# Performance work log

Hardware: AMD Instinct MI355X
Metric: run time of the kernel (lower is better)

The kernel has to match this reference:

```python
import jax, jax.numpy as jnp
import numpy as np

B, RULE_DIM, E, P, TOP_K = 8192, 128, 64, 16, 3
EPS = 1e-5
CONF_THRESH = 0.1


def _ln(x, g, b):
    # torch.nn.LayerNorm: biased variance, eps=1e-5
    m = x.mean(-1, keepdims=True)
    v = ((x - m) ** 2).mean(-1, keepdims=True)
    return (x - m) / jnp.sqrt(v + EPS) * g + b


def setup_inputs() -> dict:
    key = jax.random.key(0)
    ks = jax.random.split(key, 8)
    s = lambda fan: 1.0 / np.sqrt(fan)
    return {
        "rule_embedding": jax.random.normal(ks[0], (B, RULE_DIM), jnp.float32),
        "rp_w1": jax.random.normal(ks[1], (RULE_DIM, 256), jnp.float32) * s(RULE_DIM),
        "rp_b1": jnp.zeros((256,), jnp.float32),
        "rp_g1": jnp.ones((256,), jnp.float32),
        "rp_be1": jnp.zeros((256,), jnp.float32),
        "rp_w2": jax.random.normal(ks[2], (256, 512), jnp.float32) * s(256),
        "rp_b2": jnp.zeros((512,), jnp.float32),
        "rp_g2": jnp.ones((512,), jnp.float32),
        "rp_be2": jnp.zeros((512,), jnp.float32),
        "op_w": jax.random.normal(ks[3], (512, E), jnp.float32) * s(512),
        "op_b": jnp.zeros((E,), jnp.float32),
        "pe_w1": jax.random.normal(ks[4], (E, 512, 256), jnp.float32) * s(512),
        "pe_b1": jnp.zeros((E, 256), jnp.float32),
        "pe_g": jnp.ones((E, 256), jnp.float32),
        "pe_beta": jnp.zeros((E, 256), jnp.float32),
        "pe_w2": jax.random.normal(ks[5], (E, 256, P), jnp.float32) * s(256),
        "pe_b2": jnp.zeros((E, P), jnp.float32),
    }


def reference(rule_embedding, rp_w1, rp_b1, rp_g1, rp_be1, rp_w2, rp_b2,
              rp_g2, rp_be2, op_w, op_b, pe_w1, pe_b1, pe_g, pe_beta,
              pe_w2, pe_b2):
    # rule_parser: Linear -> LN -> ReLU -> Linear -> LN -> ReLU
    h = jax.nn.relu(_ln(rule_embedding @ rp_w1 + rp_b1, rp_g1, rp_be1))   # [B,256]
    features = jax.nn.relu(_ln(h @ rp_w2 + rp_b2, rp_g2, rp_be2))         # [B,512]

    # op routing: softmax + top-k
    op_probs = jax.nn.softmax(features @ op_w + op_b, axis=-1)            # [B,E]
    top_probs, top_idx = jax.lax.top_k(op_probs, TOP_K)                   # [B,K]

    # per-op param predictor MLP, evaluated for every expert (vmap over E)
    def expert(w1, b1, g, be, w2, b2):
        z = jax.nn.relu(_ln(features @ w1 + b1, g, be))                   # [B,256]
        return z @ w2 + b2                                                # [B,P]

    h2_all = jax.vmap(expert)(pe_w1, pe_b1, pe_g, pe_beta, pe_w2, pe_b2)  # [E,B,P]

    # gather the selected expert's raw param logits per (token, slot)
    params_sel = h2_all[top_idx, jnp.arange(B)[:, None], :]               # [B,K,P]

    # original skips ops with confidence < 0.1 -> mask them out
    mask = (top_probs >= CONF_THRESH).astype(params_sel.dtype)            # [B,K]
    params_out = params_sel * mask[..., None]

    return top_probs, top_idx, params_out
```

## Files before the change

kernel.cpp:

```cpp
#include <hip/hip_runtime.h>
#include <math.h>

#define Bv   8192
#define EPSv 1e-5f
#define CONFv 0.1f
#define MB (1024*1024)

typedef __attribute__((ext_vector_type(8))) short short8;
typedef __attribute__((ext_vector_type(4))) float f32x4;

__device__ __forceinline__ float wave_sum64(float v){
  #pragma unroll
  for (int o = 32; o; o >>= 1) v += __shfl_xor(v, o, 64);
  return v;
}

__device__ __forceinline__ void split3f(float x, short &h, short &m, short &l){
  unsigned u = __float_as_uint(x);
  h = (short)(u >> 16);
  float r1 = x - __uint_as_float(u & 0xffff0000u);
  unsigned u1 = __float_as_uint(r1);
  m = (short)(u1 >> 16);
  float r2 = r1 - __uint_as_float(u1 & 0xffff0000u);
  l = (short)(__float_as_uint(r2) >> 16);
}

__device__ __forceinline__ void split2f(float x, short &h, short &m){
  unsigned u = __float_as_uint(x);
  h = (short)(u >> 16);
  float r1 = x - __uint_as_float(u & 0xffff0000u);
  m = (short)(__float_as_uint(r1) >> 16);
}

__device__ __forceinline__ f32x4 mfma5(short8 ah, short8 am,
                                       short8 bh, short8 bm, short8 bl, f32x4 c){
  c = __builtin_amdgcn_mfma_f32_16x16x32_bf16(am, bm, c, 0, 0, 0);
  c = __builtin_amdgcn_mfma_f32_16x16x32_bf16(ah, bl, c, 0, 0, 0);
  c = __builtin_amdgcn_mfma_f32_16x16x32_bf16(am, bh, c, 0, 0, 0);
  c = __builtin_amdgcn_mfma_f32_16x16x32_bf16(ah, bm, c, 0, 0, 0);
  c = __builtin_amdgcn_mfma_f32_16x16x32_bf16(ah, bh, c, 0, 0, 0);
  return c;
}

__device__ __forceinline__ f32x4 mfma3(short8 ah, short8 al,
                                       short8 bh, short8 bl, f32x4 c){
  c = __builtin_amdgcn_mfma_f32_16x16x32_bf16(al, bh, c, 0, 0, 0);
  c = __builtin_amdgcn_mfma_f32_16x16x32_bf16(ah, bl, c, 0, 0, 0);
  c = __builtin_amdgcn_mfma_f32_16x16x32_bf16(ah, bh, c, 0, 0, 0);
  return c;
}

__global__ __launch_bounds__(256) void k_pre(
    const float* __restrict__ w1, const float* __restrict__ w2,
    const float* __restrict__ opw,
    unsigned short* __restrict__ w1p, unsigned short* __restrict__ w2p,
    unsigned short* __restrict__ opwp, int* __restrict__ cnt)
{
  int bid = blockIdx.x;
  if (bid < 128){
    int gid = bid*256 + threadIdx.x;
    int k = gid >> 8, n = gid & 255;
    short h, m, l;
    split3f(w1[gid], h, m, l);
    int idx = (((n >> 4)*4 + (k >> 5))*64 + (((k >> 3) & 3)*16 + (n & 15)))*8 + (k & 7);
    w1p[idx]             = (unsigned short)h;
    w1p[32768 + idx]     = (unsigned short)m;
    w1p[2*32768 + idx]   = (unsigned short)l;
  } else if (bid < 640){
    int gid = (bid - 128)*256 + threadIdx.x;
    int k = gid >> 9, n = gid & 511;
    short h, m, l;
    split3f(w2[gid], h, m, l);
    int idx = (((n >> 4)*8 + (k >> 5))*64 + (((k >> 3) & 3)*16 + (n & 15)))*8 + (k & 7);
    w2p[idx]             = (unsigned short)h;
    w2p[131072 + idx]    = (unsigned short)m;
    w2p[2*131072 + idx]  = (unsigned short)l;
  } else if (bid < 768){
    int gid = (bid - 640)*256 + threadIdx.x;
    int k = gid >> 6, n = gid & 63;
    short h, m, l;
    split3f(opw[gid], h, m, l);
    int idx = (((n >> 4)*16 + (k >> 5))*64 + (((k >> 3) & 3)*16 + (n & 15)))*8 + (k & 7);
    opwp[idx]            = (unsigned short)h;
    opwp[32768 + idx]    = (unsigned short)m;
    opwp[2*32768 + idx]  = (unsigned short)l;
  } else {
    if (threadIdx.x < 64) cnt[threadIdx.x] = 0;
  }
}

__global__ __launch_bounds__(1024) void k_fused(const float* __restrict__ X,
    const unsigned short* __restrict__ w1p, const float* __restrict__ b1,
    const float* __restrict__ g1, const float* __restrict__ be1,
    const unsigned short* __restrict__ w2p, const float* __restrict__ b2,
    const float* __restrict__ g2, const float* __restrict__ be2,
    const unsigned short* __restrict__ opwp, const float* __restrict__ opb,
    unsigned short* __restrict__ fh, unsigned short* __restrict__ fl,
    float* __restrict__ dout, int* __restrict__ cnt, int* __restrict__ list,
    const float* __restrict__ pw1, const float* __restrict__ pw2,
    unsigned short* __restrict__ p1, unsigned short* __restrict__ p2)
{
  extern __shared__ unsigned char smem[];

  if (blockIdx.x >= 256){
    int pb = blockIdx.x - 256;
    if (pb < 1024){
      int t = pb*1024 + threadIdx.x;
      int e = t >> 14, rem = t & 16383, kg = rem >> 8, n = rem & 255;
      const float* src = pw1 + ((size_t)e << 17) + (size_t)(kg*8)*256 + n;
      short8 h, l;
      #pragma unroll
      for (int j = 0; j < 8; j++){
        float w = src[(size_t)j*256];
        unsigned u = __float_as_uint(w);
        float r2 = w - __uint_as_float(u & 0xffff0000u);
        h[j] = (short)(u >> 16);
        l[j] = (short)(__float_as_uint(r2) >> 16);
      }
      int idx8 = ((((n >> 4)*16 + (kg >> 2))*64) + (kg & 3)*16 + (n & 15)) << 3;
      unsigned short* ep = p1 + (size_t)e * 262144;
      *(short8*)(ep + idx8)          = h;
      *(short8*)(ep + 131072 + idx8) = l;
    } else {
      int t = (pb - 1024)*1024 + threadIdx.x;
      int e = t >> 9, rem = t & 511, kg = rem >> 4, n = rem & 15;
      const float* src = pw2 + (size_t)e*4096 + (size_t)(kg*8)*16 + n;
      short8 h, l;
      #pragma unroll
      for (int j = 0; j < 8; j++){
        float w = src[(size_t)j*16];
        unsigned u = __float_as_uint(w);
        float r2 = w - __uint_as_float(u & 0xffff0000u);
        h[j] = (short)(u >> 16);
        l[j] = (short)(__float_as_uint(r2) >> 16);
      }
      int idx8 = (((kg >> 2)*64) + (kg & 3)*16 + n) << 3;
      unsigned short* ep = p2 + (size_t)e * 8192;
      *(short8*)(ep + idx8)        = h;
      *(short8*)(ep + 4096 + idx8) = l;
    }
    return;
  }

  unsigned short* xh  = (unsigned short*)smem;
  unsigned short* xm  = xh + 4096;
  unsigned short* hbh = xh + 8192;
  unsigned short* hbm = xh + 16384;
  unsigned short* gah = xh;
  unsigned short* gam = xh + 16384;
  __shared__ float ps[32][20];
  __shared__ float pq[32][20];
  __shared__ float mi[32][2];
  __shared__ float lg[32][64];

  const int tid = threadIdx.x;
  const int r0  = blockIdx.x * 32;
  const int wave = tid >> 6, lane = tid & 63, lquad = lane >> 4, l15 = lane & 15;

  {
    int r = tid >> 5, c4 = tid & 31;
    float4 v = ((const float4*)X)[(size_t)(r0+r)*32 + c4];
    unsigned u0 = __float_as_uint(v.x), u1 = __float_as_uint(v.y);
    unsigned u2 = __float_as_uint(v.z), u3 = __float_as_uint(v.w);
    float m0 = v.x - __uint_as_float(u0 & 0xffff0000u);
    float m1 = v.y - __uint_as_float(u1 & 0xffff0000u);
    float m2 = v.z - __uint_as_float(u2 & 0xffff0000u);
    float m3 = v.w - __uint_as_float(u3 & 0xffff0000u);
    unsigned hp0 = (u0 >> 16) | (u1 & 0xffff0000u);
    unsigned hp1 = (u2 >> 16) | (u3 & 0xffff0000u);
    unsigned mp0 = (__float_as_uint(m0) >> 16) | (__float_as_uint(m1) & 0xffff0000u);
    unsigned mp1 = (__float_as_uint(m2) >> 16) | (__float_as_uint(m3) & 0xffff0000u);
    int gk = c4 >> 1, half = c4 & 1;
    int off = r*128 + ((gk ^ (r & 7)) << 3) + half*4;
    ((unsigned*)(xh + off))[0] = hp0;
    ((unsigned*)(xh + off))[1] = hp1;
    ((unsigned*)(xm + off))[0] = mp0;
    ((unsigned*)(xm + off))[1] = mp1;
  }
  __syncthreads();

  float bcol1, gcol1, becol1;
  {
    int col = wave*16 + l15;
    bcol1 = b1[col]; gcol1 = g1[col]; becol1 = be1[col];
  }
  {
    f32x4 acc[2];
    acc[0] = (f32x4){0.f,0.f,0.f,0.f};
    acc[1] = (f32x4){0.f,0.f,0.f,0.f};
    const int pstride = 32768;
    for (int ks4 = 0; ks4 < 4; ks4++){
      const unsigned short* bp = w1p + (((wave*4 + ks4)*64 + lane) << 3);
      short8 bh = *(const short8*)bp;
      short8 bm = *(const short8*)(bp + pstride);
      short8 bl = *(const short8*)(bp + 2*pstride);
      #pragma unroll
      for (int mt = 0; mt < 2; mt++){
        int r = mt*16 + l15;
        int off = r*128 + (((ks4*4 + lquad) ^ (r & 7)) << 3);
        short8 ah = *(const short8*)(xh + off);
        short8 am = *(const short8*)(xm + off);
        acc[mt] = mfma5(ah, am, bh, bm, bl, acc[mt]);
      }
    }
    #pragma unroll
    for (int mt = 0; mt < 2; mt++)
      #pragma unroll
      for (int reg = 0; reg < 4; reg++){
        float z = acc[mt][reg] + bcol1;
        float s = z, q = z*z;
        #pragma unroll
        for (int o = 1; o < 16; o <<= 1){ s += __shfl_xor(s, o, 64); q += __shfl_xor(q, o, 64); }
        int row = mt*16 + lquad*4 + reg;
        if (l15 == 0){ ps[row][wave] = s; pq[row][wave] = q; }
      }
    __syncthreads();
    if (tid < 32){
      int row = tid;
      float4 s0 = *(const float4*)&ps[row][0],  s1 = *(const float4*)&ps[row][4];
      float4 s2 = *(const float4*)&ps[row][8],  s3 = *(const float4*)&ps[row][12];
      float4 q0 = *(const float4*)&pq[row][0],  q1 = *(const float4*)&pq[row][4];
      float4 q2 = *(const float4*)&pq[row][8],  q3 = *(const float4*)&pq[row][12];
      float s = s0.x; s += s0.y; s += s0.z; s += s0.w;
      s += s1.x; s += s1.y; s += s1.z; s += s1.w;
      s += s2.x; s += s2.y; s += s2.z; s += s2.w;
      s += s3.x; s += s3.y; s += s3.z; s += s3.w;
      float q = q0.x; q += q0.y; q += q0.z; q += q0.w;
      q += q1.x; q += q1.y; q += q1.z; q += q1.w;
      q += q2.x; q += q2.y; q += q2.z; q += q2.w;
      q += q3.x; q += q3.y; q += q3.z; q += q3.w;
      float mean = s * (1.0f/256.0f);
      float var  = q * (1.0f/256.0f) - mean*mean;
      mi[row][0] = mean;
      mi[row][1] = 1.0f / sqrtf(var + EPSv);
    }
    __syncthreads();
    #pragma unroll
    for (int mt = 0; mt < 2; mt++)
      #pragma unroll
      for (int reg = 0; reg < 4; reg++){
        int row = mt*16 + lquad*4 + reg;
        float2 mv = *(const float2*)mi[row];
        int col = wave*16 + l15;
        float z = acc[mt][reg] + bcol1;
        float y = fmaxf((z - mv.x)*mv.y*gcol1 + becol1, 0.f);
        short hh, mm2;
        split2f(y, hh, mm2);
        int gg = col >> 3, c7 = col & 7;
        int adr = row*256 + ((gg ^ (row & 7)) << 3) + c7;
        hbh[adr] = (unsigned short)hh;
        hbm[adr] = (unsigned short)mm2;
      }
  }
  __syncthreads();

  f32x4 acc2[2][2];
  #pragma unroll
  for (int mt = 0; mt < 2; mt++)
    #pragma unroll
    for (int nt = 0; nt < 2; nt++) acc2[mt][nt] = (f32x4){0.f,0.f,0.f,0.f};
  {
    const int pstride = 131072;
    for (int ks4 = 0; ks4 < 8; ks4++){
      short8 ah[2], am[2];
      #pragma unroll
      for (int mt = 0; mt < 2; mt++){
        int r = mt*16 + l15;
        int off = r*256 + (((ks4*4 + lquad) ^ (r & 7)) << 3);
        ah[mt] = *(const short8*)(hbh + off);
        am[mt] = *(const short8*)(hbm + off);
      }
      #pragma unroll
      for (int nt = 0; nt < 2; nt++){
        int ntg = wave*2 + nt;
        const unsigned short* bp = w2p + (((ntg*8 + ks4)*64 + lane) << 3);
        short8 bh = *(const short8*)bp;
        short8 bm = *(const short8*)(bp + pstride);
        short8 bl = *(const short8*)(bp + 2*pstride);
        #pragma unroll
        for (int mt = 0; mt < 2; mt++)
          acc2[mt][nt] = mfma5(ah[mt], am[mt], bh, bm, bl, acc2[mt][nt]);
      }
    }
  }

  float bcol[2], gcol[2], becol[2];
  #pragma unroll
  for (int nt = 0; nt < 2; nt++){
    int col = (wave*2 + nt)*16 + l15;
    bcol[nt] = b2[col]; gcol[nt] = g2[col]; becol[nt] = be2[col];
  }
  #pragma unroll
  for (int mt = 0; mt < 2; mt++)
    #pragma unroll
    for (int reg = 0; reg < 4; reg++){
      float s = 0.f, q = 0.f;
      #pragma unroll
      for (int nt = 0; nt < 2; nt++){
        float z = acc2[mt][nt][reg] + bcol[nt];
        s += z; q += z*z;
      }
      #pragma unroll
      for (int o = 1; o < 16; o <<= 1){ s += __shfl_xor(s, o, 64); q += __shfl_xor(q, o, 64); }
      int row = mt*16 + lquad*4 + reg;
      if (l15 == 0){ ps[row][wave] = s; pq[row][wave] = q; }
    }
  __syncthreads();
  if (tid < 32){
    int row = tid;
    float4 s0 = *(const float4*)&ps[row][0],  s1 = *(const float4*)&ps[row][4];
    float4 s2 = *(const float4*)&ps[row][8],  s3 = *(const float4*)&ps[row][12];
    float4 q0 = *(const float4*)&pq[row][0],  q1 = *(const float4*)&pq[row][4];
    float4 q2 = *(const float4*)&pq[row][8],  q3 = *(const float4*)&pq[row][12];
    float s = s0.x; s += s0.y; s += s0.z; s += s0.w;
    s += s1.x; s += s1.y; s += s1.z; s += s1.w;
    s += s2.x; s += s2.y; s += s2.z; s += s2.w;
    s += s3.x; s += s3.y; s += s3.z; s += s3.w;
    float q = q0.x; q += q0.y; q += q0.z; q += q0.w;
    q += q1.x; q += q1.y; q += q1.z; q += q1.w;
    q += q2.x; q += q2.y; q += q2.z; q += q2.w;
    q += q3.x; q += q3.y; q += q3.z; q += q3.w;
    float mean = s * (1.0f/512.0f);
    float var  = q * (1.0f/512.0f) - mean*mean;
    mi[row][0] = mean;
    mi[row][1] = 1.0f / sqrtf(var + EPSv);
  }
  __syncthreads();

  #pragma unroll
  for (int mt = 0; mt < 2; mt++)
    #pragma unroll
    for (int reg = 0; reg < 4; reg++){
      int row = mt*16 + lquad*4 + reg;
      float2 mv = *(const float2*)mi[row];
      #pragma unroll
      for (int nt = 0; nt < 2; nt++){
        int col = (wave*2 + nt)*16 + l15;
        float z = acc2[mt][nt][reg] + bcol[nt];
        float y = fmaxf((z - mv.x)*mv.y*gcol[nt] + becol[nt], 0.f);
        short hh, mm2;
        split2f(y, hh, mm2);
        int gg = col >> 3, c7 = col & 7;
        int adr = row*512 + ((gg ^ (row & 7)) << 3) + c7;
        gah[adr] = (unsigned short)hh;
        gam[adr] = (unsigned short)mm2;
      }
    }
  __syncthreads();

  if (wave < 4){
    f32x4 accg[2];
    accg[0] = (f32x4){0.f,0.f,0.f,0.f};
    accg[1] = (f32x4){0.f,0.f,0.f,0.f};
    for (int kt = 0; kt < 16; kt++){
      const unsigned short* bp = opwp + (((wave*16 + kt)*64 + lane) << 3);
      short8 bh = *(const short8*)bp;
      short8 bm = *(const short8*)(bp + 32768);
      short8 bl = *(const short8*)(bp + 65536);
      #pragma unroll
      for (int mt = 0; mt < 2; mt++){
        int r = mt*16 + l15;
        int off = r*512 + (((kt*4 + lquad) ^ (r & 7)) << 3);
        short8 ah = *(const short8*)(gah + off);
        short8 am = *(const short8*)(gam + off);
        accg[mt] = mfma5(ah, am, bh, bm, bl, accg[mt]);
      }
    }
    float opbv = opb[wave*16 + l15];
    #pragma unroll
    for (int mt = 0; mt < 2; mt++)
      #pragma unroll
      for (int reg = 0; reg < 4; reg++)
        lg[mt*16 + lquad*4 + reg][wave*16 + l15] = accg[mt][reg] + opbv;
  } else {
    int t4 = (wave - 4)*64 + lane;
    for (int i = t4; i < 4096; i += 768){
      int p = i >> 11, rem = i & 2047, r = rem >> 6, gg = rem & 63;
      short8 v = *(const short8*)((p ? gam : gah) + r*512 + ((gg ^ (r & 7)) << 3));
      unsigned short* dst = (p ? fl : fh) + (size_t)(r0 + r)*512 + gg*8;
      *(short8*)dst = v;
    }
  }
  __syncthreads();

  {
    for (int rr = 0; rr < 2; rr++){
      int r = wave*2 + rr, row = r0 + r;
      float l = lg[r][lane];
      float mx = l;
      #pragma unroll
      for (int o = 32; o; o >>= 1) mx = fmaxf(mx, __shfl_xor(mx, o, 64));
      float p = expf(l - mx);
      float s = wave_sum64(p);
      p /= s;
      float pv = p;
      for (int j = 0; j < 3; j++){
        float v = pv; int idx = lane;
        #pragma unroll
        for (int o = 32; o; o >>= 1){
          float ov = __shfl_xor(v, o, 64);
          int   oi = __shfl_xor(idx, o, 64);
          if (ov > v || (ov == v && oi < idx)){ v = ov; idx = oi; }
        }
        if (lane == 0){
          dout[(size_t)row*3 + j]                = v;
          dout[(size_t)Bv*3 + (size_t)row*3 + j] = (float)idx;
        }
        if (v >= CONFv){
          if (lane == 0){
            int pos = atomicAdd(&cnt[idx], 1);
            list[idx*Bv + pos] = (row << 2) | j;
          }
        } else {
          if (lane < 16) dout[(size_t)Bv*6 + (size_t)row*48 + j*16 + lane] = 0.f;
        }
        if (lane == idx) pv = -1.0f;
      }
    }
  }
}

__global__ __launch_bounds__(512) void k_expert(const unsigned short* __restrict__ fh,
    const unsigned short* __restrict__ fl,
    const unsigned short* __restrict__ p1, const float* __restrict__ b1,
    const float* __restrict__ g,  const float* __restrict__ beta,
    const unsigned short* __restrict__ p2, const float* __restrict__ b2,
    const int* __restrict__ cnt,  const int* __restrict__ list,
    float* __restrict__ dout)
{
  extern __shared__ unsigned char smem[];
  unsigned short* xh = (unsigned short*)smem;
  unsigned short* xl = xh + 32*512;
  unsigned short* zp = (unsigned short*)smem;
  __shared__ float ps[32][12];
  __shared__ float pq[32][12];
  __shared__ float mi[32][2];
  __shared__ int sdesc[3];

  const int tid = threadIdx.x;
  const int wave = tid >> 6, lane = tid & 63;
  const int lquad = lane >> 4, l15 = lane & 15;

  if (wave == 0){
    int c  = cnt[lane];
    int tl = (c + 31) >> 5;
    int incl = tl;
    #pragma unroll
    for (int o = 1; o < 64; o <<= 1){
      int v = __shfl_up(incl, o, 64);
      if (lane >= o) incl += v;
    }
    int total = __shfl(incl, 63, 64);
    int G   = (total + 7) >> 3;
    int grp = blockIdx.x & 7, rr = blockIdx.x >> 3;
    int lgc = grp*G + rr;
    int ok  = (G > 0) && (rr < G) && (lgc < total);
    unsigned long long bm = __ballot(ok && (incl > lgc));
    if (lane == 0){
      if (!ok || bm == 0ull){ sdesc[0] = -1; }
      else {
        int e = __ffsll((long long)bm) - 1;
        sdesc[0] = e; sdesc[1] = lgc; sdesc[2] = 0;
      }
    }
    if (bm != 0ull && ok){
      int e = __ffsll((long long)bm) - 1;
      int excl = __shfl(incl - tl, e, 64);
      int ne   = __shfl(c, e, 64);
      if (lane == 0){ sdesc[1] = lgc - excl; sdesc[2] = ne; }
    }
  }
  __syncthreads();
  const int e = sdesc[0];
  if (e < 0) return;
  const int t = sdesc[1];
  const int n = sdesc[2];
  const int base = t * 32;
  const int m = min(32, n - base);
  const int* lrow = list + e*Bv + base;

  for (int i = tid; i < 4096; i += 512){
    int p = i >> 11, rem = i & 2047, r = rem >> 6, gg = rem & 63;
    int ev = lrow[(r < m) ? r : 0];
    int row = ev >> 2;
    const unsigned short* src = (p ? fl : fh) + (size_t)row*512 + gg*8;
    short8 v = *(const short8*)src;
    unsigned short* dst = (p ? xl : xh) + r*512 + ((gg ^ (r & 7)) << 3);
    *(short8*)dst = v;
  }
  __syncthreads();

  const unsigned short* p1e = p1 + (size_t)e * 262144;
  f32x4 acc[2][2];
  #pragma unroll
  for (int mt = 0; mt < 2; mt++)
    #pragma unroll
    for (int nt = 0; nt < 2; nt++) acc[mt][nt] = (f32x4){0.f,0.f,0.f,0.f};

  for (int kt = 0; kt < 16; kt++){
    short8 ah[2], al[2];
    int gk = kt*4 + lquad;
    #pragma unroll
    for (int mt = 0; mt < 2; mt++){
      int r = mt*16 + l15;
      int off = r*512 + ((gk ^ (r & 7)) << 3);
      ah[mt] = *(const short8*)(xh + off);
      al[mt] = *(const short8*)(xl + off);
    }
    #pragma unroll
    for (int nt = 0; nt < 2; nt++){
      int ntg = wave*2 + nt;
      const unsigned short* bp = p1e + (((ntg*16 + kt)*64 + lane) << 3);
      short8 bh = *(const short8*)bp;
      short8 bl = *(const short8*)(bp + 131072);
      #pragma unroll
      for (int mt = 0; mt < 2; mt++)
        acc[mt][nt] = mfma3(ah[mt], al[mt], bh, bl, acc[mt][nt]);
    }
  }

  float bb[2], gv[2], bv[2];
  #pragma unroll
  for (int nt = 0; nt < 2; nt++){
    int col = (wave*2 + nt)*16 + l15;
    bb[nt] = b1[e*256 + col];
    gv[nt] = g[e*256 + col];
    bv[nt] = beta[e*256 + col];
  }
  #pragma unroll
  for (int mt = 0; mt < 2; mt++)
    #pragma unroll
    for (int reg = 0; reg < 4; reg++){
      float s = 0.f, q = 0.f;
      #pragma unroll
      for (int nt = 0; nt < 2; nt++){
        float z = acc[mt][nt][reg] + bb[nt];
        s += z; q += z*z;
      }
      #pragma unroll
      for (int o = 1; o < 16; o <<= 1){ s += __shfl_xor(s, o, 64); q += __shfl_xor(q, o, 64); }
      int row = mt*16 + lquad*4 + reg;
      if (l15 == 0){ ps[row][wave] = s; pq[row][wave] = q; }
    }
  __syncthreads();
  if (tid < 32){
    int row = tid;
    float4 s0 = *(const float4*)&ps[row][0], s1 = *(const float4*)&ps[row][4];
    float4 q0 = *(const float4*)&pq[row][0], q1 = *(const float4*)&pq[row][4];
    float s = s0.x; s += s0.y; s += s0.z; s += s0.w;
    s += s1.x; s += s1.y; s += s1.z; s += s1.w;
    float q = q0.x; q += q0.y; q += q0.z; q += q0.w;
    q += q1.x; q += q1.y; q += q1.z; q += q1.w;
    float mean = s * (1.0f/256.0f);
    float var  = q * (1.0f/256.0f) - mean*mean;
    mi[row][0] = mean;
    mi[row][1] = 1.0f / sqrtf(var + EPSv);
  }
  __syncthreads();

  #pragma unroll
  for (int mt = 0; mt < 2; mt++)
    #pragma unroll
    for (int reg = 0; reg < 4; reg++){
      int row = mt*16 + lquad*4 + reg;
      float2 mv = *(const float2*)mi[row];
      #pragma unroll
      for (int nt = 0; nt < 2; nt++){
        int col = (wave*2 + nt)*16 + l15;
        float z = acc[mt][nt][reg] + bb[nt];
        float y = fmaxf((z - mv.x)*mv.y*gv[nt] + bv[nt], 0.f);
        short hh, mm2;
        split2f(y, hh, mm2);
        zp[row*528 + col]       = (unsigned short)hh;
        zp[row*528 + 264 + col] = (unsigned short)mm2;
      }
    }
  __syncthreads();

  if (wave < 2){
    const unsigned short* p2e = p2 + (size_t)e * 8192;
    f32x4 acc2 = (f32x4){0.f,0.f,0.f,0.f};
    for (int kt2 = 0; kt2 < 8; kt2++){
      const unsigned short* zb = zp + (wave*16 + l15)*528 + kt2*32 + lquad*8;
      short8 ahh = *(const short8*)zb;
      short8 all2 = *(const short8*)(zb + 264);
      const unsigned short* bp = p2e + ((kt2*64 + lane) << 3);
      short8 bh = *(const short8*)bp;
      short8 bl = *(const short8*)(bp + 4096);
      acc2 = mfma3(ahh, all2, bh, bl, acc2);
    }
    float b2v = b2[e*16 + l15];
    #pragma unroll
    for (int reg = 0; reg < 4; reg++){
      int rl = wave*16 + lquad*4 + reg;
      if (rl < m){
        int ev = lrow[rl];
        int row = ev >> 2, j = ev & 3;
        dout[(size_t)Bv*6 + (size_t)row*48 + j*16 + l15] = acc2[reg] + b2v;
      }
    }
  }
}

extern "C" void kernel_launch(void* const* d_in, const int* in_sizes, int n_in,
                              void* d_out, int out_size, void* d_ws, size_t ws_size,
                              hipStream_t stream)
{
  const float* X   = (const float*)d_in[0];
  const float* w1  = (const float*)d_in[1];
  const float* b1  = (const float*)d_in[2];
  const float* g1  = (const float*)d_in[3];
  const float* be1 = (const float*)d_in[4];
  const float* w2  = (const float*)d_in[5];
  const float* b2  = (const float*)d_in[6];
  const float* g2  = (const float*)d_in[7];
  const float* be2 = (const float*)d_in[8];
  const float* opw = (const float*)d_in[9];
  const float* opb = (const float*)d_in[10];
  const float* pw1 = (const float*)d_in[11];
  const float* pb1 = (const float*)d_in[12];
  const float* pg  = (const float*)d_in[13];
  const float* pbe = (const float*)d_in[14];
  const float* pw2 = (const float*)d_in[15];
  const float* pb2 = (const float*)d_in[16];
  float* out = (float*)d_out;
  char*  ws  = (char*)d_ws;

  unsigned short* p1E    = (unsigned short*)ws;
  unsigned short* p2E    = (unsigned short*)(ws + (size_t)32*MB);
  unsigned short* w1p_rp = (unsigned short*)(ws + (size_t)33*MB);
  unsigned short* w2p_rp = (unsigned short*)(ws + (size_t)34*MB);
  unsigned short* opwp   = (unsigned short*)(ws + (size_t)35*MB);
  unsigned short* fh     = (unsigned short*)(ws + (size_t)36*MB);
  unsigned short* fl     = (unsigned short*)(ws + (size_t)44*MB);
  int*            list   = (int*)(ws + (size_t)52*MB);
  int*            cnt    = (int*)(ws + (size_t)54*MB);

  k_pre   <<<769, 256, 0, stream>>>(w1, w2, opw, w1p_rp, w2p_rp, opwp, cnt);
  k_fused <<<1312, 1024, 65536, stream>>>(X, w1p_rp, b1, g1, be1,
                                          w2p_rp, b2, g2, be2, opwp, opb,
                                          fh, fl, out, cnt, list,
                                          pw1, pw2, p1E, p2E);
  k_expert<<<832,  512, 65536, stream>>>(fh, fl, p1E, pb1, pg, pbe, p2E, pb2,
                                         cnt, list, out);
}
```

Before: 169.9 us.

## Double-buffer expert weight loads, add nontemporal packing and priority hints

Software-pipelines the expert layer-1 B-operand global loads with two register buffers so the next k-step's weights load while the current MFMAs run. It also makes the weight-packing blocks use nontemporal loads and stores, raises wave priority for the compute blocks, and fully unrolls the gather and second-layer loops. The aim is to hide global load latency in the expert GEMM. The cost is higher register pressure, which may lower occupancy.

```diff
diff --git a/kernel.cpp b/kernel.cpp
--- a/kernel.cpp
+++ b/kernel.cpp
@@ -111,7 +111,7 @@
       short8 h, l;
       #pragma unroll
       for (int j = 0; j < 8; j++){
-        float w = src[(size_t)j*256];
+        float w = __builtin_nontemporal_load(src + (size_t)j*256);
         unsigned u = __float_as_uint(w);
         float r2 = w - __uint_as_float(u & 0xffff0000u);
         h[j] = (short)(u >> 16);
@@ -119,8 +119,8 @@
       }
       int idx8 = ((((n >> 4)*16 + (kg >> 2))*64) + (kg & 3)*16 + (n & 15)) << 3;
       unsigned short* ep = p1 + (size_t)e * 262144;
-      *(short8*)(ep + idx8)          = h;
-      *(short8*)(ep + 131072 + idx8) = l;
+      __builtin_nontemporal_store(h, (short8*)(ep + idx8));
+      __builtin_nontemporal_store(l, (short8*)(ep + 131072 + idx8));
     } else {
       int t = (pb - 1024)*1024 + threadIdx.x;
       int e = t >> 9, rem = t & 511, kg = rem >> 4, n = rem & 15;
@@ -128,7 +128,7 @@
       short8 h, l;
       #pragma unroll
       for (int j = 0; j < 8; j++){
-        float w = src[(size_t)j*16];
+        float w = __builtin_nontemporal_load(src + (size_t)j*16);
         unsigned u = __float_as_uint(w);
         float r2 = w - __uint_as_float(u & 0xffff0000u);
         h[j] = (short)(u >> 16);
@@ -136,11 +136,13 @@
       }
       int idx8 = (((kg >> 2)*64) + (kg & 3)*16 + n) << 3;
       unsigned short* ep = p2 + (size_t)e * 8192;
-      *(short8*)(ep + idx8)        = h;
-      *(short8*)(ep + 4096 + idx8) = l;
+      __builtin_nontemporal_store(h, (short8*)(ep + idx8));
+      __builtin_nontemporal_store(l, (short8*)(ep + 4096 + idx8));
     }
     return;
   }
+
+  __builtin_amdgcn_s_setprio(1);
 
   unsigned short* xh  = (unsigned short*)smem;
   unsigned short* xm  = xh + 4096;
@@ -479,6 +481,7 @@
   const int m = min(32, n - base);
   const int* lrow = list + e*Bv + base;
 
+  #pragma unroll
   for (int i = tid; i < 4096; i += 512){
     int p = i >> 11, rem = i & 2047, r = rem >> 6, gg = rem & 63;
     int ev = lrow[(r < m) ? r : 0];
@@ -491,33 +494,51 @@
   __syncthreads();
 
   const unsigned short* p1e = p1 + (size_t)e * 262144;
+  const unsigned short* bB = p1e + wave*16384 + lane*8;
   f32x4 acc[2][2];
   #pragma unroll
   for (int mt = 0; mt < 2; mt++)
     #pragma unroll
     for (int nt = 0; nt < 2; nt++) acc[mt][nt] = (f32x4){0.f,0.f,0.f,0.f};
 
-  for (int kt = 0; kt < 16; kt++){
-    short8 ah[2], al[2];
-    int gk = kt*4 + lquad;
-    #pragma unroll
-    for (int mt = 0; mt < 2; mt++){
-      int r = mt*16 + l15;
-      int off = r*512 + ((gk ^ (r & 7)) << 3);
-      ah[mt] = *(const short8*)(xh + off);
-      al[mt] = *(const short8*)(xl + off);
-    }
-    #pragma unroll
-    for (int nt = 0; nt < 2; nt++){
-      int ntg = wave*2 + nt;
-      const unsigned short* bp = p1e + (((ntg*16 + kt)*64 + lane) << 3);
-      short8 bh = *(const short8*)bp;
-      short8 bl = *(const short8*)(bp + 131072);
-      #pragma unroll
-      for (int mt = 0; mt < 2; mt++)
-        acc[mt][nt] = mfma3(ah[mt], al[mt], bh, bl, acc[mt][nt]);
-    }
-  }
+#define LOADB(KT, BH, BL) do { \
+  _Pragma("unroll") \
+  for (int nt = 0; nt < 2; nt++){ \
+    const unsigned short* bp = bB + nt*8192 + (KT)*512; \
+    BH[nt] = *(const short8*)bp; \
+    BL[nt] = *(const short8*)(bp + 131072); \
+  } } while(0)
+
+#define COMPK(KT, BH, BL) do { \
+  short8 ah[2], al[2]; \
+  int gk = (KT)*4 + lquad; \
+  _Pragma("unroll") \
+  for (int mt = 0; mt < 2; mt++){ \
+    int r = mt*16 + l15; \
+    int off = r*512 + ((gk ^ (r & 7)) << 3); \
+    ah[mt] = *(const short8*)(xh + off); \
+    al[mt] = *(const short8*)(xl + off); \
+  } \
+  _Pragma("unroll") \
+  for (int nt = 0; nt < 2; nt++) \
+    _Pragma("unroll") \
+    for (int mt = 0; mt < 2; mt++) \
+      acc[mt][nt] = mfma3(ah[mt], al[mt], BH[nt], BL[nt], acc[mt][nt]); \
+  } while(0)
+
+  {
+    short8 bhA[2], blA[2], bhB[2], blB[2];
+    LOADB(0, bhA, blA);
+    #pragma unroll
+    for (int kt = 0; kt < 16; kt += 2){
+      LOADB(kt+1, bhB, blB);
+      COMPK(kt, bhA, blA);
+      if (kt + 2 < 16) LOADB(kt+2, bhA, blA);
+      COMPK(kt+1, bhB, blB);
+    }
+  }
+#undef LOADB
+#undef COMPK
 
   float bb[2], gv[2], bv[2];
   #pragma unroll
@@ -580,6 +601,7 @@
   if (wave < 2){
     const unsigned short* p2e = p2 + (size_t)e * 8192;
     f32x4 acc2 = (f32x4){0.f,0.f,0.f,0.f};
+    #pragma unroll
     for (int kt2 = 0; kt2 < 8; kt2++){
       const unsigned short* zb = zp + (wave*16 + l15)*528 + kt2*32 + lquad*8;
       short8 ahh = *(const short8*)zb;
```

New measurement: 178.1 us. 1.05x slower.
